# Kernel optimization log

Hardware: AMD Instinct MI355X
Metric: run time of the kernel (lower is better)

## Reference

```python
import jax, jax.numpy as jnp
import numpy as np

B, S, D, H = 2, 2048, 1024, 16
HD = D // H  # head_dim = 64


def setup_inputs() -> dict:
    key = jax.random.key(0)
    ks = jax.random.split(key, 11)
    init = 1.0 / np.sqrt(D)
    inp = {
        "query": jax.random.normal(ks[0], (B, S, D), jnp.float32),
        "key": jax.random.normal(ks[1], (B, S, D), jnp.float32),
        "value": jax.random.normal(ks[2], (B, S, D), jnp.float32),
        "Wq": jax.random.uniform(ks[3], (D, D), jnp.float32, -init, init),
        "bq": jax.random.uniform(ks[4], (D,), jnp.float32, -init, init),
        "Wk": jax.random.uniform(ks[5], (D, D), jnp.float32, -init, init),
        "bk": jax.random.uniform(ks[6], (D,), jnp.float32, -init, init),
        "Wv": jax.random.uniform(ks[7], (D, D), jnp.float32, -init, init),
        "bv": jax.random.uniform(ks[8], (D,), jnp.float32, -init, init),
        "Wo": jax.random.uniform(ks[9], (D, D), jnp.float32, -init, init),
        "bo": jax.random.uniform(ks[10], (D,), jnp.float32, -init, init),
    }
    return inp


def reference(query, key, value, Wq, bq, Wk, bk, Wv, bv, Wo, bo):
    # Linear projections (torch Linear: x @ W.T + b)
    q = query @ Wq.T + bq  # [B,S,D]
    k = key @ Wk.T + bk
    v = value @ Wv.T + bv
    # split heads -> [B,H,S,HD]
    q = q.reshape(B, S, H, HD).transpose(0, 2, 1, 3)
    k = k.reshape(B, S, H, HD).transpose(0, 2, 1, 3)
    v = v.reshape(B, S, H, HD).transpose(0, 2, 1, 3)
    # NOTE: original code divides by scale = head_dim**-0.5, i.e. multiplies
    # scores by sqrt(head_dim). Reproduced faithfully.
    scale = HD ** (-0.5)
    scores = jnp.einsum("bhqd,bhkd->bhqk", q, k) / scale  # [B,H,S,S]
    attn = jax.nn.softmax(scores, axis=-1)
    x = jnp.einsum("bhqk,bhkd->bhqd", attn, v)  # [B,H,S,HD]
    x = x.transpose(0, 2, 1, 3).reshape(B, S, D)
    return x @ Wo.T + bo
```

## Files before the change

### kernel.cpp

```cpp
#include <hip/hip_runtime.h>
#include <stdint.h>
#include <stddef.h>

#define SCALE_LOG2E 11.541560327111707f
#define E8 4194304
#define M1 1048576
#define NROW 65536

typedef __attribute__((ext_vector_type(8))) _Float16 f16x8;
typedef __attribute__((ext_vector_type(4))) _Float16 f16x4;
typedef __attribute__((ext_vector_type(4))) float f32x4;

#if __has_builtin(__builtin_amdgcn_exp2f)
#define EXP2F(x) __builtin_amdgcn_exp2f(x)
#else
#define EXP2F(x) exp2f(x)
#endif

__device__ __forceinline__ f32x4 mfma_f16(f16x8 a, f16x8 b, f32x4 c) {
  return __builtin_amdgcn_mfma_f32_16x16x32_f16(a, b, c, 0, 0, 0);
}

__device__ __forceinline__ void async16(const void* g, void* lds) {
  __builtin_amdgcn_global_load_lds(
      (const __attribute__((address_space(1))) unsigned int*)g,
      (__attribute__((address_space(3))) unsigned int*)lds, 16, 0, 0);
}

__global__ void prep_all(const float* __restrict__ q, const float* __restrict__ k,
                         const float* __restrict__ v,
                         const float* __restrict__ wq, const float* __restrict__ wk,
                         const float* __restrict__ wv, const float* __restrict__ wo,
                         _Float16* __restrict__ Xf, _Float16* __restrict__ Wf) {
  const int gid = blockIdx.x;
  const float* src;
  _Float16* dst;
  int i;
  if (gid < 12288) {
    const int z = gid >> 12;
    src = (z == 0) ? q : (z == 1) ? k : v;
    dst = Xf + (size_t)z * E8;
    i = (gid & 4095) * 256 + threadIdx.x;
  } else {
    const int g2 = gid - 12288;
    const int z = g2 >> 10;
    src = (z == 0) ? wq : (z == 1) ? wk : (z == 2) ? wv : wo;
    dst = Wf + (size_t)z * M1;
    i = (g2 & 1023) * 256 + threadIdx.x;
  }
  float4 x = ((const float4*)src)[i];
  f16x4 h = {(_Float16)x.x, (_Float16)x.y, (_Float16)x.z, (_Float16)x.w};
  ((f16x4*)dst)[i] = h;
}

__global__ __launch_bounds__(256, 3) void gemm_qkv(
    const _Float16* __restrict__ Xf,
    const _Float16* __restrict__ Wf,
    const float* __restrict__ bq, const float* __restrict__ bk,
    const float* __restrict__ bv,
    _Float16* __restrict__ Of)
{
  __shared__ _Float16 SMEM[16384];
  _Float16* LA = SMEM;
  _Float16* LB = SMEM + 8192;
  const int z = blockIdx.z;
  const int tid = threadIdx.x;
  const int lane = tid & 63;
  const int wv = tid >> 6;
  const int wm = wv >> 1, wn = wv & 1;
  const int rl = lane & 15, qd = lane >> 4;
  const int m0 = blockIdx.y * 128, n0 = blockIdx.x * 128;

  const _Float16* A0 = Xf + (size_t)z * E8;
  const _Float16* W0 = Wf + (size_t)z * M1;
  const float* bias = (z == 0) ? bq : (z == 1) ? bk : bv;

  f32x4 acc[4][4];
#pragma unroll
  for (int i = 0; i < 4; i++)
#pragma unroll
    for (int j = 0; j < 4; j++) acc[i][j] = f32x4{0.f, 0.f, 0.f, 0.f};

  const int srow = wv * 32 + (lane >> 2);
  const int scol = (lane & 3) * 8;

  auto stage = [&](int k0, int buf) {
    const _Float16* ga = A0 + (size_t)(m0 + srow) * 1024 + k0 + scol;
    async16(ga, &LA[buf * 4096 + wv * 1024]);
    async16(ga + 16 * 1024, &LA[buf * 4096 + wv * 1024 + 512]);
    const _Float16* gb = W0 + (size_t)(n0 + srow) * 1024 + k0 + scol;
    async16(gb, &LB[buf * 4096 + wv * 1024]);
    async16(gb + 16 * 1024, &LB[buf * 4096 + wv * 1024 + 512]);
  };

  stage(0, 0);
  for (int t = 0; t < 32; t++) {
    const int buf = t & 1;
    __syncthreads();
    if (t + 1 < 32) stage((t + 1) * 32, buf ^ 1);
    f16x8 af[4], bfr[4];
#pragma unroll
    for (int i = 0; i < 4; i++) af[i] = *(const f16x8*)&LA[buf * 4096 + (wm * 64 + i * 16 + rl) * 32 + qd * 8];
#pragma unroll
    for (int j = 0; j < 4; j++) bfr[j] = *(const f16x8*)&LB[buf * 4096 + (wn * 64 + j * 16 + rl) * 32 + qd * 8];
#pragma unroll
    for (int i = 0; i < 4; i++)
#pragma unroll
      for (int j = 0; j < 4; j++) acc[i][j] = mfma_f16(af[i], bfr[j], acc[i][j]);
  }

  if (z == 2) {
#pragma unroll
    for (int j = 0; j < 4; j++) {
      const int nn = n0 + wn * 64 + j * 16 + rl;
      const float bj = bias[nn];
      const int hh = nn >> 6, e = nn & 63;
#pragma unroll
      for (int i = 0; i < 4; i++) {
        const int mm = m0 + wm * 64 + i * 16 + qd * 4;
        const int b = mm >> 11, s = mm & 2047;
        f16x4 pk = {(_Float16)(acc[i][j][0] + bj), (_Float16)(acc[i][j][1] + bj),
                    (_Float16)(acc[i][j][2] + bj), (_Float16)(acc[i][j][3] + bj)};
        *(f16x4*)(Of + 2 * (size_t)E8 + (((size_t)((b * 16 + hh) * 64 + e)) << 11) + s) = pk;
      }
    }
  } else {
    const float scl = (z == 0) ? SCALE_LOG2E : 1.0f;
    _Float16* base = Of + (size_t)z * E8;
    __syncthreads();
#pragma unroll
    for (int j = 0; j < 4; j++) {
      const int nl = wn * 64 + j * 16 + rl;
      const float bj = bias[n0 + nl];
#pragma unroll
      for (int i = 0; i < 4; i++) {
        const int ml = wm * 64 + i * 16 + qd * 4;
        const int np = nl ^ (qd << 4);
#pragma unroll
        for (int r = 0; r < 4; r++)
          SMEM[(ml + r) * 128 + np] = (_Float16)((acc[i][j][r] + bj) * scl);
      }
    }
    __syncthreads();
#pragma unroll
    for (int it2 = 0; it2 < 8; it2++) {
      const int m = (it2 * 256 + tid) >> 4;
      const int col8 = (tid & 15) * 8;
      const int np = col8 ^ (((m >> 2) & 3) << 4);
      f16x8 vrow = *(const f16x8*)&SMEM[m * 128 + np];
      const int sg = m0 + m;
      const int b = sg >> 11, s = sg & 2047;
      const int nn = n0 + col8;
      const int hh = nn >> 6, e = nn & 63;
      *(f16x8*)(base + (((size_t)((b * 16 + hh) * 2048 + s)) << 6) + e) = vrow;
    }
  }
}

__global__ __launch_bounds__(256, 3) void attn_kernel(
    const _Float16* __restrict__ Qb,
    const _Float16* __restrict__ Kb,
    const _Float16* __restrict__ Vt,
    float* __restrict__ Op,
    float2* __restrict__ ML)
{
  __shared__ _Float16 Ks[2][4096];
  __shared__ _Float16 Vs[2][4096];
  __shared__ _Float16 Ps[4][32][76];
  const int tid = threadIdx.x;
  const int lane = tid & 63;
  const int wv = tid >> 6;
  const int rl = lane & 15, qd = lane >> 4;
  const int bh = blockIdx.z;
  const int half = blockIdx.y;
  const int kvb = half * 1024;
  const int q0 = blockIdx.x * 128 + wv * 32;

  f16x8 qf[2][2];
#pragma unroll
  for (int mt = 0; mt < 2; mt++)
#pragma unroll
    for (int kk = 0; kk < 2; kk++)
      qf[mt][kk] = *(const f16x8*)(Qb + ((size_t)bh * 2048 + q0 + mt * 16 + rl) * 64 +
                                   kk * 32 + qd * 8);

  float m_[2] = {-1e30f, -1e30f}, l_[2] = {0.f, 0.f};
  f32x4 o[2][4];
#pragma unroll
  for (int mt = 0; mt < 2; mt++)
#pragma unroll
    for (int jt = 0; jt < 4; jt++) o[mt][jt] = f32x4{0.f, 0.f, 0.f, 0.f};

  auto stage = [&](int kv, int buf) {
#pragma unroll
    for (int it = 0; it < 2; it++) {
      const int cI = it * 256 + tid;
      const int row = cI >> 3;
      const int c = (cI & 7) ^ (row & 7);
      const int dst = (it * 256 + wv * 64) * 8;
      async16(Kb + ((size_t)bh * 2048 + kv + row) * 64 + c * 8, &Ks[buf][dst]);
      async16(Vt + ((size_t)bh * 64 + row) * 2048 + kv + c * 8, &Vs[buf][dst]);
    }
  };

  stage(kvb, 0);

  for (int t = 0; t < 16; t++) {
    const int buf = t & 1;
    __syncthreads();
    if (t + 1 < 16) stage(kvb + (t + 1) * 64, buf ^ 1);

    f32x4 sc[2][4];
#pragma unroll
    for (int mt = 0; mt < 2; mt++)
#pragma unroll
      for (int nt = 0; nt < 4; nt++) sc[mt][nt] = f32x4{0.f, 0.f, 0.f, 0.f};
#pragma unroll
    for (int nt = 0; nt < 4; nt++) {
      const int ro = (nt * 16 + rl) * 64;
#pragma unroll
      for (int kk = 0; kk < 2; kk++) {
        const int cc = (((kk * 4 + qd) ^ (rl & 7)) << 3);
        f16x8 kh = *(const f16x8*)&Ks[buf][ro + cc];
#pragma unroll
        for (int mt = 0; mt < 2; mt++)
          sc[mt][nt] = mfma_f16(kh, qf[mt][kk], sc[mt][nt]);
      }
    }

#pragma unroll
    for (int mt = 0; mt < 2; mt++) {
      float mloc = sc[mt][0][0];
#pragma unroll
      for (int nt = 0; nt < 4; nt++)
#pragma unroll
        for (int r = 0; r < 4; r++) mloc = fmaxf(mloc, sc[mt][nt][r]);
      float mx = fmaxf(mloc, __shfl_xor(mloc, 16));
      mx = fmaxf(mx, __shfl_xor(mx, 32));
      float sm = 0.f;
#pragma unroll
      for (int nt = 0; nt < 4; nt++)
#pragma unroll
        for (int r = 0; r < 4; r++) {
          float p = EXP2F(sc[mt][nt][r] - mloc);
          sc[mt][nt][r] = p;
          sm += p;
        }
      const float mold = m_[mt];
      const float mnew = fmaxf(mold, mx);
      m_[mt] = mnew;
      const float cf = EXP2F(mloc - mnew);
      if (__any(mnew > mold)) {
        const float al = EXP2F(mold - mnew);
        l_[mt] = l_[mt] * al + sm * cf;
#pragma unroll
        for (int jt = 0; jt < 4; jt++)
#pragma unroll
          for (int r = 0; r < 4; r++) o[mt][jt][r] *= al;
      } else {
        l_[mt] += sm * cf;
      }

#pragma unroll
      for (int nt = 0; nt < 4; nt++) {
        f16x4 pk = {(_Float16)(sc[mt][nt][0] * cf), (_Float16)(sc[mt][nt][1] * cf),
                    (_Float16)(sc[mt][nt][2] * cf), (_Float16)(sc[mt][nt][3] * cf)};
        *(f16x4*)&Ps[wv][mt * 16 + rl][nt * 16 + qd * 4] = pk;
      }
    }

#pragma unroll
    for (int kk2 = 0; kk2 < 2; kk2++) {
      f16x8 pf[2];
#pragma unroll
      for (int mt = 0; mt < 2; mt++)
        pf[mt] = *(const f16x8*)&Ps[wv][mt * 16 + rl][kk2 * 32 + qd * 8];
#pragma unroll
      for (int jt = 0; jt < 4; jt++) {
        const int cc = (((kk2 * 4 + qd) ^ (rl & 7)) << 3);
        f16x8 vv = *(const f16x8*)&Vs[buf][(jt * 16 + rl) * 64 + cc];
#pragma unroll
        for (int mt = 0; mt < 2; mt++)
          o[mt][jt] = mfma_f16(vv, pf[mt], o[mt][jt]);
      }
    }
  }

#pragma unroll
  for (int mt = 0; mt < 2; mt++) {
    float lt = l_[mt] + __shfl_xor(l_[mt], 16);
    lt += __shfl_xor(lt, 32);
    const size_t row = (size_t)bh * 2048 + q0 + mt * 16 + rl;
    float* op = Op + ((size_t)half * NROW + row) * 64;
#pragma unroll
    for (int jt = 0; jt < 4; jt++)
      *(f32x4*)(op + jt * 16 + qd * 4) = o[mt][jt];
    if (qd == 0) ML[(size_t)half * NROW + row] = make_float2(m_[mt], lt);
  }
}

__global__ void merge_kernel(const float* __restrict__ Op,
                             const float2* __restrict__ ML,
                             _Float16* __restrict__ Xo) {
  const int t = threadIdx.x;
  const int row = blockIdx.x * 16 + (t >> 4);
  const int d0 = (t & 15) * 4;
  const float2 ml1 = ML[row];
  const float2 ml2 = ML[NROW + row];
  const float m = fmaxf(ml1.x, ml2.x);
  const float w1 = EXP2F(ml1.x - m), w2 = EXP2F(ml2.x - m);
  const float inv = 1.0f / (ml1.y * w1 + ml2.y * w2);
  const float4 o1 = *(const float4*)(Op + (size_t)row * 64 + d0);
  const float4 o2 = *(const float4*)(Op + (size_t)NROW * 64 + (size_t)row * 64 + d0);
  const int bh = row >> 11, q = row & 2047;
  const int b = bh >> 4, hh = bh & 15;
  f16x4 pk = {(_Float16)((o1.x * w1 + o2.x * w2) * inv),
              (_Float16)((o1.y * w1 + o2.y * w2) * inv),
              (_Float16)((o1.z * w1 + o2.z * w2) * inv),
              (_Float16)((o1.w * w1 + o2.w * w2) * inv)};
  *(f16x4*)(Xo + ((size_t)(b * 2048 + q)) * 1024 + hh * 64 + d0) = pk;
}

__global__ __launch_bounds__(256, 2) void gemm_out(
    const _Float16* __restrict__ A0,
    const _Float16* __restrict__ W0,
    const float* __restrict__ bias,
    float* __restrict__ out)
{
  __shared__ _Float16 LA[2][2048];
  __shared__ _Float16 LB[2][4096];
  const int tid = threadIdx.x;
  const int lane = tid & 63;
  const int wv = tid >> 6;
  const int wm = wv >> 1, wn = wv & 1;
  const int rl = lane & 15, qd = lane >> 4;
  const int m0 = blockIdx.y * 64, n0 = blockIdx.x * 128;

  f32x4 acc[2][4];
#pragma unroll
  for (int i = 0; i < 2; i++)
#pragma unroll
    for (int j = 0; j < 4; j++) acc[i][j] = f32x4{0.f, 0.f, 0.f, 0.f};

  auto stage = [&](int k0, int buf) {
    {
      const int row = tid >> 2, c = tid & 3;
      async16(A0 + (size_t)(m0 + row) * 1024 + k0 + c * 8, &LA[buf][wv * 512]);
    }
#pragma unroll
    for (int it = 0; it < 2; it++) {
      const int cI = it * 256 + tid;
      const int row = cI >> 2, c = cI & 3;
      async16(W0 + (size_t)(n0 + row) * 1024 + k0 + c * 8,
              &LB[buf][it * 2048 + wv * 512]);
    }
  };

  stage(0, 0);
  for (int t = 0; t < 32; t++) {
    const int buf = t & 1;
    __syncthreads();
    if (t + 1 < 32) stage((t + 1) * 32, buf ^ 1);
    f16x8 af[2], bfr[4];
#pragma unroll
    for (int i = 0; i < 2; i++) af[i] = *(const f16x8*)&LA[buf][(wm * 32 + i * 16 + rl) * 32 + qd * 8];
#pragma unroll
    for (int j = 0; j < 4; j++) bfr[j] = *(const f16x8*)&LB[buf][(wn * 64 + j * 16 + rl) * 32 + qd * 8];
#pragma unroll
    for (int i = 0; i < 2; i++)
#pragma unroll
      for (int j = 0; j < 4; j++) acc[i][j] = mfma_f16(af[i], bfr[j], acc[i][j]);
  }

#pragma unroll
  for (int j = 0; j < 4; j++) {
    const int nn = n0 + wn * 64 + j * 16 + rl;
    const float bj = bias[nn];
#pragma unroll
    for (int i = 0; i < 2; i++) {
      const int mm = m0 + wm * 32 + i * 16 + qd * 4;
#pragma unroll
      for (int r = 0; r < 4; r++)
        out[(size_t)(mm + r) * 1024 + nn] = acc[i][j][r] + bj;
    }
  }
}

extern "C" void kernel_launch(void* const* d_in, const int* in_sizes, int n_in,
                              void* d_out, int out_size, void* d_ws, size_t ws_size,
                              hipStream_t stream) {
  const float* query = (const float*)d_in[0];
  const float* key   = (const float*)d_in[1];
  const float* value = (const float*)d_in[2];
  const float* Wq = (const float*)d_in[3];
  const float* bq = (const float*)d_in[4];
  const float* Wk = (const float*)d_in[5];
  const float* bk = (const float*)d_in[6];
  const float* Wv = (const float*)d_in[7];
  const float* bv = (const float*)d_in[8];
  const float* Wo = (const float*)d_in[9];
  const float* bo = (const float*)d_in[10];

  _Float16* ws = (_Float16*)d_ws;
  _Float16* Xf = ws;
  _Float16* Wf = ws + 3 * (size_t)E8;
  _Float16* Qh = Wf + 4 * (size_t)M1;
  _Float16* Kh = Qh + (size_t)E8;
  _Float16* Vt = Kh + (size_t)E8;
  _Float16* Xa = Vt + (size_t)E8;
  float*    Op = (float*)(Xa + (size_t)E8);
  float2*   ML = (float2*)(Op + 2 * (size_t)NROW * 64);

  prep_all<<<16384, 256, 0, stream>>>(query, key, value, Wq, Wk, Wv, Wo, Xf, Wf);
  gemm_qkv<<<dim3(8, 32, 3), 256, 0, stream>>>(Xf, Wf, bq, bk, bv, Qh);
  attn_kernel<<<dim3(16, 2, 32), 256, 0, stream>>>(Qh, Kh, Vt, Op, ML);
  merge_kernel<<<4096, 256, 0, stream>>>(Op, ML, Xa);
  gemm_out<<<dim3(8, 64), 256, 0, stream>>>(Xa, Wf + 3 * (size_t)M1, bo, (float*)d_out);
}
```

Baseline: 245.7 us.

## Transpose P via ds_bpermute instead of LDS, store partial outputs in fp16

The attention kernel no longer writes the softmax probabilities to a shared-memory scratch tile. Instead it packs them into registers and rearranges them across lanes with ds_bpermute to form the MFMA B operand. This frees LDS, so launch bounds go from 3 to 4 blocks per CU. The split-KV partial outputs are now stored in fp16 instead of fp32, which halves the write and read traffic between the attention and merge kernels at some cost in precision. The softmax max and sum reductions are also rewritten as balanced trees.

```diff
diff --git a/kernel.cpp b/kernel.cpp
--- a/kernel.cpp
+++ b/kernel.cpp
@@ -26,6 +26,12 @@
       (const __attribute__((address_space(1))) unsigned int*)g,
       (__attribute__((address_space(3))) unsigned int*)lds, 16, 0, 0);
 }
+
+__device__ __forceinline__ unsigned int hbits(_Float16 h) {
+  return (unsigned int)__builtin_bit_cast(unsigned short, h);
+}
+
+typedef union { unsigned int u[4]; f16x8 h; } PU;
 
 __global__ void prep_all(const float* __restrict__ q, const float* __restrict__ k,
                          const float* __restrict__ v,
@@ -157,16 +163,15 @@
   }
 }
 
-__global__ __launch_bounds__(256, 3) void attn_kernel(
+__global__ __launch_bounds__(256, 4) void attn_kernel(
     const _Float16* __restrict__ Qb,
     const _Float16* __restrict__ Kb,
     const _Float16* __restrict__ Vt,
-    float* __restrict__ Op,
+    _Float16* __restrict__ Op,
     float2* __restrict__ ML)
 {
   __shared__ _Float16 Ks[2][4096];
   __shared__ _Float16 Vs[2][4096];
-  __shared__ _Float16 Ps[4][32][76];
   const int tid = threadIdx.x;
   const int lane = tid & 63;
   const int wv = tid >> 6;
@@ -176,6 +181,10 @@
   const int kvb = half * 1024;
   const int q0 = blockIdx.x * 128 + wv * 32;
 
+  const int alo = ((((qd & 1) << 5) + rl) << 2);
+  const int ahi = alo + 64;
+  const bool selA = (qd < 2);
+
   f16x8 qf[2][2];
 #pragma unroll
   for (int mt = 0; mt < 2; mt++)
@@ -228,24 +237,29 @@
       }
     }
 
+    unsigned int pw[2][4][2];
 #pragma unroll
     for (int mt = 0; mt < 2; mt++) {
-      float mloc = sc[mt][0][0];
+      float tm[4];
 #pragma unroll
       for (int nt = 0; nt < 4; nt++)
-#pragma unroll
-        for (int r = 0; r < 4; r++) mloc = fmaxf(mloc, sc[mt][nt][r]);
+        tm[nt] = fmaxf(fmaxf(sc[mt][nt][0], sc[mt][nt][1]),
+                       fmaxf(sc[mt][nt][2], sc[mt][nt][3]));
+      float mloc = fmaxf(fmaxf(tm[0], tm[1]), fmaxf(tm[2], tm[3]));
       float mx = fmaxf(mloc, __shfl_xor(mloc, 16));
       mx = fmaxf(mx, __shfl_xor(mx, 32));
-      float sm = 0.f;
-#pragma unroll
-      for (int nt = 0; nt < 4; nt++)
-#pragma unroll
-        for (int r = 0; r < 4; r++) {
-          float p = EXP2F(sc[mt][nt][r] - mloc);
-          sc[mt][nt][r] = p;
-          sm += p;
-        }
+      float ts[4];
+#pragma unroll
+      for (int nt = 0; nt < 4; nt++) {
+        float p0 = EXP2F(sc[mt][nt][0] - mloc);
+        float p1 = EXP2F(sc[mt][nt][1] - mloc);
+        float p2 = EXP2F(sc[mt][nt][2] - mloc);
+        float p3 = EXP2F(sc[mt][nt][3] - mloc);
+        sc[mt][nt][0] = p0; sc[mt][nt][1] = p1;
+        sc[mt][nt][2] = p2; sc[mt][nt][3] = p3;
+        ts[nt] = (p0 + p1) + (p2 + p3);
+      }
+      const float sm = (ts[0] + ts[1]) + (ts[2] + ts[3]);
       const float mold = m_[mt];
       const float mnew = fmaxf(mold, mx);
       m_[mt] = mnew;
@@ -260,12 +274,14 @@
       } else {
         l_[mt] += sm * cf;
       }
-
 #pragma unroll
       for (int nt = 0; nt < 4; nt++) {
-        f16x4 pk = {(_Float16)(sc[mt][nt][0] * cf), (_Float16)(sc[mt][nt][1] * cf),
-                    (_Float16)(sc[mt][nt][2] * cf), (_Float16)(sc[mt][nt][3] * cf)};
-        *(f16x4*)&Ps[wv][mt * 16 + rl][nt * 16 + qd * 4] = pk;
+        _Float16 h0 = (_Float16)(sc[mt][nt][0] * cf);
+        _Float16 h1 = (_Float16)(sc[mt][nt][1] * cf);
+        _Float16 h2 = (_Float16)(sc[mt][nt][2] * cf);
+        _Float16 h3 = (_Float16)(sc[mt][nt][3] * cf);
+        pw[mt][nt][0] = hbits(h0) | (hbits(h1) << 16);
+        pw[mt][nt][1] = hbits(h2) | (hbits(h3) << 16);
       }
     }
 
@@ -273,8 +289,31 @@
     for (int kk2 = 0; kk2 < 2; kk2++) {
       f16x8 pf[2];
 #pragma unroll
-      for (int mt = 0; mt < 2; mt++)
-        pf[mt] = *(const f16x8*)&Ps[wv][mt * 16 + rl][kk2 * 32 + qd * 8];
+      for (int mt = 0; mt < 2; mt++) {
+        const int na = kk2 * 2, nb = na + 1;
+        PU pu;
+        {
+          unsigned int a = __builtin_amdgcn_ds_bpermute(alo, (int)pw[mt][na][0]);
+          unsigned int b = __builtin_amdgcn_ds_bpermute(alo, (int)pw[mt][nb][0]);
+          pu.u[0] = selA ? a : b;
+        }
+        {
+          unsigned int a = __builtin_amdgcn_ds_bpermute(alo, (int)pw[mt][na][1]);
+          unsigned int b = __builtin_amdgcn_ds_bpermute(alo, (int)pw[mt][nb][1]);
+          pu.u[1] = selA ? a : b;
+        }
+        {
+          unsigned int a = __builtin_amdgcn_ds_bpermute(ahi, (int)pw[mt][na][0]);
+          unsigned int b = __builtin_amdgcn_ds_bpermute(ahi, (int)pw[mt][nb][0]);
+          pu.u[2] = selA ? a : b;
+        }
+        {
+          unsigned int a = __builtin_amdgcn_ds_bpermute(ahi, (int)pw[mt][na][1]);
+          unsigned int b = __builtin_amdgcn_ds_bpermute(ahi, (int)pw[mt][nb][1]);
+          pu.u[3] = selA ? a : b;
+        }
+        pf[mt] = pu.h;
+      }
 #pragma unroll
       for (int jt = 0; jt < 4; jt++) {
         const int cc = (((kk2 * 4 + qd) ^ (rl & 7)) << 3);
@@ -291,15 +330,18 @@
     float lt = l_[mt] + __shfl_xor(l_[mt], 16);
     lt += __shfl_xor(lt, 32);
     const size_t row = (size_t)bh * 2048 + q0 + mt * 16 + rl;
-    float* op = Op + ((size_t)half * NROW + row) * 64;
-#pragma unroll
-    for (int jt = 0; jt < 4; jt++)
-      *(f32x4*)(op + jt * 16 + qd * 4) = o[mt][jt];
+    _Float16* op = Op + ((size_t)half * NROW + row) * 64;
+#pragma unroll
+    for (int jt = 0; jt < 4; jt++) {
+      f16x4 pk = {(_Float16)o[mt][jt][0], (_Float16)o[mt][jt][1],
+                  (_Float16)o[mt][jt][2], (_Float16)o[mt][jt][3]};
+      *(f16x4*)(op + jt * 16 + qd * 4) = pk;
+    }
     if (qd == 0) ML[(size_t)half * NROW + row] = make_float2(m_[mt], lt);
   }
 }
 
-__global__ void merge_kernel(const float* __restrict__ Op,
+__global__ void merge_kernel(const _Float16* __restrict__ Op,
                              const float2* __restrict__ ML,
                              _Float16* __restrict__ Xo) {
   const int t = threadIdx.x;
@@ -310,14 +352,14 @@
   const float m = fmaxf(ml1.x, ml2.x);
   const float w1 = EXP2F(ml1.x - m), w2 = EXP2F(ml2.x - m);
   const float inv = 1.0f / (ml1.y * w1 + ml2.y * w2);
-  const float4 o1 = *(const float4*)(Op + (size_t)row * 64 + d0);
-  const float4 o2 = *(const float4*)(Op + (size_t)NROW * 64 + (size_t)row * 64 + d0);
+  f16x4 o1 = *(const f16x4*)(Op + (size_t)row * 64 + d0);
+  f16x4 o2 = *(const f16x4*)(Op + (size_t)NROW * 64 + (size_t)row * 64 + d0);
   const int bh = row >> 11, q = row & 2047;
   const int b = bh >> 4, hh = bh & 15;
-  f16x4 pk = {(_Float16)((o1.x * w1 + o2.x * w2) * inv),
-              (_Float16)((o1.y * w1 + o2.y * w2) * inv),
-              (_Float16)((o1.z * w1 + o2.z * w2) * inv),
-              (_Float16)((o1.w * w1 + o2.w * w2) * inv)};
+  f16x4 pk = {(_Float16)(((float)o1[0] * w1 + (float)o2[0] * w2) * inv),
+              (_Float16)(((float)o1[1] * w1 + (float)o2[1] * w2) * inv),
+              (_Float16)(((float)o1[2] * w1 + (float)o2[2] * w2) * inv),
+              (_Float16)(((float)o1[3] * w1 + (float)o2[3] * w2) * inv)};
   *(f16x4*)(Xo + ((size_t)(b * 2048 + q)) * 1024 + hh * 64 + d0) = pk;
 }
 
@@ -408,7 +450,7 @@
   _Float16* Kh = Qh + (size_t)E8;
   _Float16* Vt = Kh + (size_t)E8;
   _Float16* Xa = Vt + (size_t)E8;
-  float*    Op = (float*)(Xa + (size_t)E8);
+  _Float16* Op = Xa + (size_t)E8;
   float2*   ML = (float2*)(Op + 2 * (size_t)NROW * 64);
 
   prep_all<<<16384, 256, 0, stream>>>(query, key, value, Wq, Wk, Wv, Wo, Xf, Wf);
```

After: 253.6 us. 1.03x slower.
